# Kernel optimization log

Measured on AMD Instinct MI355X. Metric: run time of the kernel, lower is better.

The kernel has to match this reference:

```python
import jax, jax.numpy as jnp
import numpy as np

N = 100_000      # num nodes
E = 100_000      # num hyperedges
NNZ = 1_600_000  # incidence entries (avg degree 16)
DIN = 128
DOUT = 128


def setup_inputs() -> dict:
    key = jax.random.key(0)
    k1, k2, k3, k4 = jax.random.split(key, 4)
    x = jax.random.normal(k1, (N, DIN), dtype=jnp.float32)
    weight = jax.random.normal(k2, (DIN, DOUT), dtype=jnp.float32) / np.sqrt(DIN).astype(np.float32)
    bias = jax.random.normal(k3, (DOUT,), dtype=jnp.float32) * 0.02
    hyperedge_index = jax.random.randint(k4, (2, NNZ), 0, N, dtype=jnp.int64)
    return {"x": x, "weight": weight, "bias": bias, "hyperedge_index": hyperedge_index}


def reference(x, weight, bias, hyperedge_index):
    # PyG HypergraphConv (use_attention=False, heads=1):
    #   out = D^{-1} H W B^{-1} H^T (x @ Theta) + bias, W = I (unit hyperedge weights)
    node_idx = hyperedge_index[0]  # [NNZ]
    edge_idx = hyperedge_index[1]  # [NNZ]

    h = x @ weight  # [N, DOUT]

    ones = jnp.ones((NNZ,), dtype=h.dtype)
    # node degree D_i = sum of hyperedge weights (=1) over incident hyperedges
    D = jax.ops.segment_sum(ones, node_idx, num_segments=N)   # [N]
    # hyperedge degree B_e = number of incident nodes
    B = jax.ops.segment_sum(ones, edge_idx, num_segments=E)   # [E]
    Dinv = jnp.where(D > 0, 1.0 / D, 0.0)
    Binv = jnp.where(B > 0, 1.0 / B, 0.0)

    # nodes -> hyperedges: m_e = B_e^{-1} * sum_{i in e} h_i
    e_feat = jax.ops.segment_sum(h[node_idx], edge_idx, num_segments=E) * Binv[:, None]  # [E, DOUT]
    # hyperedges -> nodes: out_i = D_i^{-1} * sum_{e ni i} m_e
    out = jax.ops.segment_sum(e_feat[edge_idx], node_idx, num_segments=N) * Dinv[:, None]  # [N, DOUT]
    return out + bias
```

## Files before the change

### kernel.cpp

```cpp
#include <hip/hip_runtime.h>

#define Nn 100000
#define Ne 100000
#define NNZC 1600000
#define NBLK 256
#define CHUNK 6250
#define BSH 8
#define BUCKW 256
#define NBK 391
#define GEMM_BLOCKS 1563

typedef __attribute__((ext_vector_type(8))) short short8;
typedef __attribute__((ext_vector_type(4))) float floatx4;

__device__ inline unsigned short f2bf(float f) {
    union { float f; unsigned int i; } c; c.f = f;
    unsigned int i = c.i;
    return (unsigned short)((i + 0x7fffu + ((i >> 16) & 1u)) >> 16);
}
__device__ inline unsigned int f2bf2(float lo, float hi) {
    union { float f; unsigned int i; } a, b;
    a.f = lo; b.f = hi;
    const unsigned int x = (a.i + 0x7fffu + ((a.i >> 16) & 1u)) >> 16;
    const unsigned int y = (b.i + 0x7fffu + ((b.i >> 16) & 1u)) & 0xffff0000u;
    return x | y;
}

__global__ void hist_kernel(const int* __restrict__ nidx, const int* __restrict__ eidx,
                            int* __restrict__ histN, int* __restrict__ histE) {
    __shared__ int hN[NBK], hE[NBK];
    for (int j = threadIdx.x; j < NBK; j += 256) { hN[j] = 0; hE[j] = 0; }
    __syncthreads();
    const int base = blockIdx.x * CHUNK;
    for (int i = base + threadIdx.x; i < base + CHUNK; i += 256) {
        atomicAdd(&hN[nidx[i] >> BSH], 1);
        atomicAdd(&hE[eidx[i] >> BSH], 1);
    }
    __syncthreads();
    for (int j = threadIdx.x; j < NBK; j += 256) {
        histN[j * NBLK + blockIdx.x] = hN[j];
        histE[j * NBLK + blockIdx.x] = hE[j];
    }
}

__global__ void scan1_kernel(int* __restrict__ histN, int* __restrict__ histE,
                             int* __restrict__ bsumN, int* __restrict__ bsumE) {
    const int arr = blockIdx.x / NBK;
    const int b = blockIdx.x % NBK;
    int* a = arr ? histE : histN;
    int* bs = arr ? bsumE : bsumN;
    const int t = threadIdx.x;
    int v = a[b * 256 + t];
    __shared__ int tmp[2][256];
    int pin = 0;
    tmp[0][t] = v;
    for (int off = 1; off < 256; off <<= 1) {
        __syncthreads();
        int val = tmp[pin][t];
        if (t >= off) val += tmp[pin][t - off];
        tmp[1 - pin][t] = val;
        pin ^= 1;
    }
    __syncthreads();
    int incl = tmp[pin][t];
    a[b * 256 + t] = incl - v;
    if (t == 255) bs[b] = incl;
}

__global__ void scan3_kernel(int* __restrict__ histN, int* __restrict__ histE,
                             const int* __restrict__ bsumN, const int* __restrict__ bsumE) {
    const int arr = blockIdx.x / NBK;
    const int b = blockIdx.x % NBK;
    int* a = arr ? histE : histN;
    const int* bs = arr ? bsumE : bsumN;
    const int t = threadIdx.x;
    int part = 0;
    for (int i = t; i < b; i += 256) part += bs[i];
    __shared__ int red[256];
    red[t] = part;
    __syncthreads();
    for (int off = 128; off > 0; off >>= 1) {
        if (t < off) red[t] += red[t + off];
        __syncthreads();
    }
    a[b * 256 + t] += red[0];
}

__global__ __launch_bounds__(256) void gemm_scatter_kernel(
        const float* __restrict__ x, const float* __restrict__ w,
        unsigned short* __restrict__ h,
        const int* __restrict__ nidx, const int* __restrict__ eidx,
        const int* __restrict__ histN, const int* __restrict__ histE,
        unsigned int* __restrict__ pairsN, unsigned int* __restrict__ pairsE) {
    __shared__ union {
        struct { unsigned short wlds[128 * 136]; unsigned short tile[4][16 * 136]; } g;
        struct { int cN[NBK]; int cE[NBK]; } s;
    } sm;
    const int tid = threadIdx.x;

    if (blockIdx.x < GEMM_BLOCKS) {
        const int wave = tid >> 6, lane = tid & 63;
        const int q = lane >> 4, r16 = lane & 15;

        for (int i = tid; i < 4096; i += 256) {
            const int k = i >> 5;
            const int n0 = (i & 31) << 2;
            const float4 wv = *(const float4*)(w + k * 128 + n0);
            sm.g.wlds[(n0 + 0) * 136 + k] = f2bf(wv.x);
            sm.g.wlds[(n0 + 1) * 136 + k] = f2bf(wv.y);
            sm.g.wlds[(n0 + 2) * 136 + k] = f2bf(wv.z);
            sm.g.wlds[(n0 + 3) * 136 + k] = f2bf(wv.w);
        }
        __syncthreads();

        const int row0 = blockIdx.x * 64 + wave * 16;
        if (row0 >= Nn) return;

        floatx4 acc[8];
#pragma unroll
        for (int jb = 0; jb < 8; ++jb) acc[jb] = (floatx4){0.f, 0.f, 0.f, 0.f};

        const float* ap = x + (size_t)(row0 + r16) * 128 + q * 8;
#pragma unroll
        for (int kk = 0; kk < 4; ++kk) {
            const float4 a0 = *(const float4*)(ap + kk * 32);
            const float4 a1 = *(const float4*)(ap + kk * 32 + 4);
            union { unsigned int u[4]; short8 s; } af;
            af.u[0] = f2bf2(a0.x, a0.y);
            af.u[1] = f2bf2(a0.z, a0.w);
            af.u[2] = f2bf2(a1.x, a1.y);
            af.u[3] = f2bf2(a1.z, a1.w);
            const unsigned short* wp = sm.g.wlds + kk * 32 + q * 8;
#pragma unroll
            for (int jb = 0; jb < 8; ++jb) {
                const short8 bfr = *(const short8*)(wp + (jb * 16 + r16) * 136);
                acc[jb] = __builtin_amdgcn_mfma_f32_16x16x32_bf16(af.s, bfr, acc[jb], 0, 0, 0);
            }
        }

        unsigned short* tw = sm.g.tile[wave];
#pragma unroll
        for (int jb = 0; jb < 8; ++jb)
#pragma unroll
            for (int r = 0; r < 4; ++r)
                tw[(q * 4 + r) * 136 + jb * 16 + r16] = f2bf(acc[jb][r]);

        const int rr = lane >> 2, seg = lane & 3;
        const unsigned short* src = tw + rr * 136 + seg * 32;
        unsigned short* dst = h + (size_t)(row0 + rr) * 128 + seg * 32;
        *(short8*)(dst + 0)  = *(const short8*)(src + 0);
        *(short8*)(dst + 8)  = *(const short8*)(src + 8);
        *(short8*)(dst + 16) = *(const short8*)(src + 16);
        *(short8*)(dst + 24) = *(const short8*)(src + 24);
    } else {
        const int blk = blockIdx.x - GEMM_BLOCKS;
        for (int j = tid; j < NBK; j += 256) {
            sm.s.cN[j] = histN[j * NBLK + blk];
            sm.s.cE[j] = histE[j * NBLK + blk];
        }
        __syncthreads();
        const int base = blk * CHUNK;
        for (int i = base + tid; i < base + CHUNK; i += 256) {
            const int n = nidx[i], e = eidx[i];
            const int pn = atomicAdd(&sm.s.cN[n >> BSH], 1);
            const int pe = atomicAdd(&sm.s.cE[e >> BSH], 1);
            pairsN[pn] = ((unsigned int)e << 8) | (unsigned int)(n & 255);
            pairsE[pe] = ((unsigned int)n << 8) | (unsigned int)(e & 255);
        }
    }
}

__global__ void fine_kernel(const unsigned int* __restrict__ pairsN, const unsigned int* __restrict__ pairsE,
                            const int* __restrict__ histN, const int* __restrict__ histE,
                            int* __restrict__ offsN, int* __restrict__ offsE,
                            int* __restrict__ permN, int* __restrict__ permE) {
    const int arr = blockIdx.x / NBK;
    const int b = blockIdx.x % NBK;
    const unsigned int* pairs = arr ? pairsE : pairsN;
    const int* hist = arr ? histE : histN;
    int* offs = arr ? offsE : offsN;
    int* perm = arr ? permE : permN;
    const int t = threadIdx.x;
    const int S = hist[b * NBLK];
    const int E = (b + 1 < NBK) ? hist[(b + 1) * NBLK] : NNZC;
    __shared__ int cnt[BUCKW];
    __shared__ int tmp[2][BUCKW];
    cnt[t] = 0;
    __syncthreads();
    for (int i = S + t; i < E; i += BUCKW)
        atomicAdd(&cnt[pairs[i] & 255u], 1);
    __syncthreads();
    int v = cnt[t];
    int pin = 0;
    tmp[0][t] = v;
    for (int off = 1; off < BUCKW; off <<= 1) {
        __syncthreads();
        int val = tmp[pin][t];
        if (t >= off) val += tmp[pin][t - off];
        tmp[1 - pin][t] = val;
        pin ^= 1;
    }
    __syncthreads();
    const int excl = tmp[pin][t] - v;
    const int id = b * BUCKW + t;
    if (id < 100000) offs[id] = S + excl;
    if (b == NBK - 1 && t == 0) offs[100000] = NNZC;
    __syncthreads();
    cnt[t] = excl;
    __syncthreads();
    for (int i = S + t; i < E; i += BUCKW) {
        const unsigned int p = pairs[i];
        const int pos = S + atomicAdd(&cnt[p & 255u], 1);
        perm[pos] = (int)(p >> 8);
    }
}

__device__ inline void gather_rows(const char* __restrict__ src, const int* __restrict__ perm,
                                   int start, int end, int lane, float& ax, float& ay) {
    const unsigned int laneoff = (unsigned int)lane << 2;
    for (int s0 = start; s0 < end; s0 += 64) {
        const int m = min(end - s0, 64);
        const int myv = perm[s0 + (lane < m ? lane : 0)];
        int t = 0;
        for (; t + 7 < m; t += 8) {
            unsigned int a[8], u[8];
#pragma unroll
            for (int j = 0; j < 8; ++j)
                a[j] = ((unsigned int)__shfl(myv, t + j, 64) << 8) | laneoff;
#pragma unroll
            for (int j = 0; j < 8; ++j) u[j] = *(const unsigned int*)(src + a[j]);
#pragma unroll
            for (int j = 0; j < 8; ++j) {
                ax += __uint_as_float(u[j] << 16);
                ay += __uint_as_float(u[j] & 0xffff0000u);
            }
        }
        if (t < m) {
            unsigned int a[8], u[8];
            float f[8];
#pragma unroll
            for (int j = 0; j < 8; ++j) {
                const int idx = (t + j < m) ? t + j : t;
                f[j] = (t + j < m) ? 1.f : 0.f;
                a[j] = ((unsigned int)__shfl(myv, idx, 64) << 8) | laneoff;
            }
#pragma unroll
            for (int j = 0; j < 8; ++j) u[j] = *(const unsigned int*)(src + a[j]);
#pragma unroll
            for (int j = 0; j < 8; ++j) {
                ax += f[j] * __uint_as_float(u[j] << 16);
                ay += f[j] * __uint_as_float(u[j] & 0xffff0000u);
            }
        }
    }
}

__global__ void gather_n2e_kernel(const int* __restrict__ perm, const int* __restrict__ offs,
                                  const unsigned short* __restrict__ h,
                                  unsigned short* __restrict__ ef) {
    const int wave = threadIdx.x >> 6;
    const int lane = threadIdx.x & 63;
    const int e = blockIdx.x * 4 + wave;
    const int start = offs[e], end = offs[e + 1];
    float ax = 0.f, ay = 0.f;
    gather_rows((const char*)h, perm, start, end, lane, ax, ay);
    const int deg = end - start;
    const float binv = deg ? 1.f / (float)deg : 0.f;
    const unsigned int o = f2bf2(ax * binv, ay * binv);
    *(unsigned int*)((char*)ef + (((unsigned int)e << 8) | ((unsigned int)lane << 2))) = o;
}

__global__ void gather_e2n_kernel(const int* __restrict__ perm, const int* __restrict__ offs,
                                  const unsigned short* __restrict__ ef,
                                  const float* __restrict__ bias,
                                  float* __restrict__ out) {
    const int wave = threadIdx.x >> 6;
    const int lane = threadIdx.x & 63;
    const int n = blockIdx.x * 4 + wave;
    const int start = offs[n], end = offs[n + 1];
    float ax = 0.f, ay = 0.f;
    gather_rows((const char*)ef, perm, start, end, lane, ax, ay);
    const int deg = end - start;
    const float dinv = deg ? 1.f / (float)deg : 0.f;
    const float2 b = ((const float2*)bias)[lane];
    float2 o;
    o.x = ax * dinv + b.x;
    o.y = ay * dinv + b.y;
    *(float2*)((char*)out + (((unsigned int)n << 9) | ((unsigned int)lane << 3))) = o;
}

extern "C" void kernel_launch(void* const* d_in, const int* in_sizes, int n_in,
                              void* d_out, int out_size, void* d_ws, size_t ws_size,
                              hipStream_t stream) {
    const float* x = (const float*)d_in[0];
    const float* w = (const float*)d_in[1];
    const float* bias = (const float*)d_in[2];
    const int* hei = (const int*)d_in[3];
    const int* nidx = hei;
    const int* eidx = hei + NNZC;
    float* out = (float*)d_out;

    char* p = (char*)d_ws;
    unsigned short* h = (unsigned short*)p;  p += (size_t)Nn * 128 * 2;
    unsigned short* ef = (unsigned short*)p; p += (size_t)Ne * 128 * 2;
    int* histN = (int*)p;                    p += (size_t)NBK * NBLK * 4 + 256;
    int* histE = (int*)p;                    p += (size_t)NBK * NBLK * 4 + 256;
    int* bsumN = (int*)p;                    p += 1792;
    int* bsumE = (int*)p;                    p += 1792;
    int* offsN = (int*)p;                    p += 400128;
    int* offsE = (int*)p;                    p += 400128;
    int* permN = (int*)p;                    p += (size_t)NNZC * 4;
    int* permE = (int*)p;                    p += (size_t)NNZC * 4;
    unsigned int* pairsN = (unsigned int*)p; p += (size_t)NNZC * 4;
    unsigned int* pairsE = (unsigned int*)p; p += (size_t)NNZC * 4;

    hist_kernel<<<NBLK, 256, 0, stream>>>(nidx, eidx, histN, histE);
    scan1_kernel<<<2 * NBK, 256, 0, stream>>>(histN, histE, bsumN, bsumE);
    scan3_kernel<<<2 * NBK, 256, 0, stream>>>(histN, histE, bsumN, bsumE);
    gemm_scatter_kernel<<<GEMM_BLOCKS + NBLK, 256, 0, stream>>>(
        x, w, h, nidx, eidx, histN, histE, pairsN, pairsE);
    fine_kernel<<<2 * NBK, BUCKW, 0, stream>>>(pairsN, pairsE, histN, histE,
                                               offsN, offsE, permN, permE);

    gather_n2e_kernel<<<Ne / 4, 256, 0, stream>>>(permE, offsE, h, ef);
    gather_e2n_kernel<<<Nn / 4, 256, 0, stream>>>(permN, offsN, ef, bias, out);
}
```

Measured before the change: 313.1 us.

## Split GEMM across histogram and scatter kernels, cache bucket pairs in LDS

The GEMM blocks are now split in half. One half runs alongside the histogram pass and the other alongside the scatter pass, so the light memory-bound kernels overlap with compute. The GEMM epilogue swaps MFMA operand order and writes bf16 results straight to global memory, dropping the LDS transpose tile and shrinking shared memory. The fine sort kernel caches the bucket's pairs in LDS on its first pass so the second pass avoids reloading them from global memory, at the cost of more LDS per block.

After: 299.8 us. -4.2%, faster.

```diff
diff --git a/kernel.cpp b/kernel.cpp
--- a/kernel.cpp
+++ b/kernel.cpp
@@ -8,7 +8,10 @@
 #define BSH 8
 #define BUCKW 256
 #define NBK 391
-#define GEMM_BLOCKS 1563
+#define GEMM_TOTAL 1563
+#define GEMM_A 782
+#define GEMM_B 781
+#define FCAP 5888
 
 typedef __attribute__((ext_vector_type(8))) short short8;
 typedef __attribute__((ext_vector_type(4))) float floatx4;
@@ -26,20 +29,88 @@
     return x | y;
 }
 
-__global__ void hist_kernel(const int* __restrict__ nidx, const int* __restrict__ eidx,
-                            int* __restrict__ histN, int* __restrict__ histE) {
-    __shared__ int hN[NBK], hE[NBK];
-    for (int j = threadIdx.x; j < NBK; j += 256) { hN[j] = 0; hE[j] = 0; }
-    __syncthreads();
-    const int base = blockIdx.x * CHUNK;
-    for (int i = base + threadIdx.x; i < base + CHUNK; i += 256) {
-        atomicAdd(&hN[nidx[i] >> BSH], 1);
-        atomicAdd(&hE[eidx[i] >> BSH], 1);
-    }
-    __syncthreads();
-    for (int j = threadIdx.x; j < NBK; j += 256) {
-        histN[j * NBLK + blockIdx.x] = hN[j];
-        histE[j * NBLK + blockIdx.x] = hE[j];
+union FusedLds {
+    unsigned short wlds[128 * 136];
+    struct { int a[NBK]; int b[NBK]; } s;
+};
+
+__device__ inline void gemm_block(int gb, const float* __restrict__ x,
+                                  const float* __restrict__ w,
+                                  unsigned short* __restrict__ h,
+                                  unsigned short* wlds, int tid) {
+    const int wave = tid >> 6, lane = tid & 63;
+    const int q = lane >> 4, r16 = lane & 15;
+
+    for (int i = tid; i < 4096; i += 256) {
+        const int k = i >> 5;
+        const int n0 = (i & 31) << 2;
+        const float4 wv = *(const float4*)(w + k * 128 + n0);
+        wlds[(n0 + 0) * 136 + k] = f2bf(wv.x);
+        wlds[(n0 + 1) * 136 + k] = f2bf(wv.y);
+        wlds[(n0 + 2) * 136 + k] = f2bf(wv.z);
+        wlds[(n0 + 3) * 136 + k] = f2bf(wv.w);
+    }
+    __syncthreads();
+
+    const int row0 = gb * 64 + wave * 16;
+    const int rrow = min(row0 + r16, Nn - 1);
+
+    floatx4 acc[8];
+#pragma unroll
+    for (int jb = 0; jb < 8; ++jb) acc[jb] = (floatx4){0.f, 0.f, 0.f, 0.f};
+
+    const float* ap = x + (size_t)rrow * 128 + q * 8;
+#pragma unroll
+    for (int kk = 0; kk < 4; ++kk) {
+        const float4 a0 = *(const float4*)(ap + kk * 32);
+        const float4 a1 = *(const float4*)(ap + kk * 32 + 4);
+        union { unsigned int u[4]; short8 s; } xf;
+        xf.u[0] = f2bf2(a0.x, a0.y);
+        xf.u[1] = f2bf2(a0.z, a0.w);
+        xf.u[2] = f2bf2(a1.x, a1.y);
+        xf.u[3] = f2bf2(a1.z, a1.w);
+        const unsigned short* wp = wlds + kk * 32 + q * 8;
+#pragma unroll
+        for (int jb = 0; jb < 8; ++jb) {
+            const short8 wf = *(const short8*)(wp + (jb * 16 + r16) * 136);
+            acc[jb] = __builtin_amdgcn_mfma_f32_16x16x32_bf16(wf, xf.s, acc[jb], 0, 0, 0);
+        }
+    }
+
+    if (row0 + r16 < Nn) {
+        unsigned short* hb = h + (size_t)(row0 + r16) * 128 + q * 4;
+#pragma unroll
+        for (int jb = 0; jb < 8; ++jb) {
+            uint2 o;
+            o.x = f2bf2(acc[jb][0], acc[jb][1]);
+            o.y = f2bf2(acc[jb][2], acc[jb][3]);
+            *(uint2*)(hb + jb * 16) = o;
+        }
+    }
+}
+
+__global__ __launch_bounds__(256) void hist_gemm_kernel(
+        const int* __restrict__ nidx, const int* __restrict__ eidx,
+        int* __restrict__ histN, int* __restrict__ histE,
+        const float* __restrict__ x, const float* __restrict__ w,
+        unsigned short* __restrict__ h) {
+    __shared__ FusedLds sm;
+    const int tid = threadIdx.x;
+    if (blockIdx.x < NBLK) {
+        for (int j = tid; j < NBK; j += 256) { sm.s.a[j] = 0; sm.s.b[j] = 0; }
+        __syncthreads();
+        const int base = blockIdx.x * CHUNK;
+        for (int i = base + tid; i < base + CHUNK; i += 256) {
+            atomicAdd(&sm.s.a[nidx[i] >> BSH], 1);
+            atomicAdd(&sm.s.b[eidx[i] >> BSH], 1);
+        }
+        __syncthreads();
+        for (int j = tid; j < NBK; j += 256) {
+            histN[j * NBLK + blockIdx.x] = sm.s.a[j];
+            histE[j * NBLK + blockIdx.x] = sm.s.b[j];
+        }
+    } else {
+        gemm_block(blockIdx.x - NBLK, x, w, h, sm.wlds, tid);
     }
 }
 
@@ -86,87 +157,31 @@
     a[b * 256 + t] += red[0];
 }
 
-__global__ __launch_bounds__(256) void gemm_scatter_kernel(
-        const float* __restrict__ x, const float* __restrict__ w,
-        unsigned short* __restrict__ h,
+__global__ __launch_bounds__(256) void scatter_gemm_kernel(
         const int* __restrict__ nidx, const int* __restrict__ eidx,
         const int* __restrict__ histN, const int* __restrict__ histE,
-        unsigned int* __restrict__ pairsN, unsigned int* __restrict__ pairsE) {
-    __shared__ union {
-        struct { unsigned short wlds[128 * 136]; unsigned short tile[4][16 * 136]; } g;
-        struct { int cN[NBK]; int cE[NBK]; } s;
-    } sm;
+        unsigned int* __restrict__ pairsN, unsigned int* __restrict__ pairsE,
+        const float* __restrict__ x, const float* __restrict__ w,
+        unsigned short* __restrict__ h) {
+    __shared__ FusedLds sm;
     const int tid = threadIdx.x;
-
-    if (blockIdx.x < GEMM_BLOCKS) {
-        const int wave = tid >> 6, lane = tid & 63;
-        const int q = lane >> 4, r16 = lane & 15;
-
-        for (int i = tid; i < 4096; i += 256) {
-            const int k = i >> 5;
-            const int n0 = (i & 31) << 2;
-            const float4 wv = *(const float4*)(w + k * 128 + n0);
-            sm.g.wlds[(n0 + 0) * 136 + k] = f2bf(wv.x);
-            sm.g.wlds[(n0 + 1) * 136 + k] = f2bf(wv.y);
-            sm.g.wlds[(n0 + 2) * 136 + k] = f2bf(wv.z);
-            sm.g.wlds[(n0 + 3) * 136 + k] = f2bf(wv.w);
-        }
-        __syncthreads();
-
-        const int row0 = blockIdx.x * 64 + wave * 16;
-        if (row0 >= Nn) return;
-
-        floatx4 acc[8];
-#pragma unroll
-        for (int jb = 0; jb < 8; ++jb) acc[jb] = (floatx4){0.f, 0.f, 0.f, 0.f};
-
-        const float* ap = x + (size_t)(row0 + r16) * 128 + q * 8;
-#pragma unroll
-        for (int kk = 0; kk < 4; ++kk) {
-            const float4 a0 = *(const float4*)(ap + kk * 32);
-            const float4 a1 = *(const float4*)(ap + kk * 32 + 4);
-            union { unsigned int u[4]; short8 s; } af;
-            af.u[0] = f2bf2(a0.x, a0.y);
-            af.u[1] = f2bf2(a0.z, a0.w);
-            af.u[2] = f2bf2(a1.x, a1.y);
-            af.u[3] = f2bf2(a1.z, a1.w);
-            const unsigned short* wp = sm.g.wlds + kk * 32 + q * 8;
-#pragma unroll
-            for (int jb = 0; jb < 8; ++jb) {
-                const short8 bfr = *(const short8*)(wp + (jb * 16 + r16) * 136);
-                acc[jb] = __builtin_amdgcn_mfma_f32_16x16x32_bf16(af.s, bfr, acc[jb], 0, 0, 0);
-            }
-        }
-
-        unsigned short* tw = sm.g.tile[wave];
-#pragma unroll
-        for (int jb = 0; jb < 8; ++jb)
-#pragma unroll
-            for (int r = 0; r < 4; ++r)
-                tw[(q * 4 + r) * 136 + jb * 16 + r16] = f2bf(acc[jb][r]);
-
-        const int rr = lane >> 2, seg = lane & 3;
-        const unsigned short* src = tw + rr * 136 + seg * 32;
-        unsigned short* dst = h + (size_t)(row0 + rr) * 128 + seg * 32;
-        *(short8*)(dst + 0)  = *(const short8*)(src + 0);
-        *(short8*)(dst + 8)  = *(const short8*)(src + 8);
-        *(short8*)(dst + 16) = *(const short8*)(src + 16);
-        *(short8*)(dst + 24) = *(const short8*)(src + 24);
-    } else {
-        const int blk = blockIdx.x - GEMM_BLOCKS;
+    if (blockIdx.x < NBLK) {
+        const int blk = blockIdx.x;
         for (int j = tid; j < NBK; j += 256) {
-            sm.s.cN[j] = histN[j * NBLK + blk];
-            sm.s.cE[j] = histE[j * NBLK + blk];
+            sm.s.a[j] = histN[j * NBLK + blk];
+            sm.s.b[j] = histE[j * NBLK + blk];
         }
         __syncthreads();
         const int base = blk * CHUNK;
         for (int i = base + tid; i < base + CHUNK; i += 256) {
             const int n = nidx[i], e = eidx[i];
-            const int pn = atomicAdd(&sm.s.cN[n >> BSH], 1);
-            const int pe = atomicAdd(&sm.s.cE[e >> BSH], 1);
+            const int pn = atomicAdd(&sm.s.a[n >> BSH], 1);
+            const int pe = atomicAdd(&sm.s.b[e >> BSH], 1);
             pairsN[pn] = ((unsigned int)e << 8) | (unsigned int)(n & 255);
             pairsE[pe] = ((unsigned int)n << 8) | (unsigned int)(e & 255);
         }
+    } else {
+        gemm_block(GEMM_A + blockIdx.x - NBLK, x, w, h, sm.wlds, tid);
     }
 }
 
@@ -185,10 +200,15 @@
     const int E = (b + 1 < NBK) ? hist[(b + 1) * NBLK] : NNZC;
     __shared__ int cnt[BUCKW];
     __shared__ int tmp[2][BUCKW];
+    __shared__ unsigned int cache[FCAP];
     cnt[t] = 0;
     __syncthreads();
-    for (int i = S + t; i < E; i += BUCKW)
-        atomicAdd(&cnt[pairs[i] & 255u], 1);
+    for (int i = S + t; i < E; i += BUCKW) {
+        const unsigned int p = pairs[i];
+        const int loc = i - S;
+        if (loc < FCAP) cache[loc] = p;
+        atomicAdd(&cnt[p & 255u], 1);
+    }
     __syncthreads();
     int v = cnt[t];
     int pin = 0;
@@ -209,7 +229,8 @@
     cnt[t] = excl;
     __syncthreads();
     for (int i = S + t; i < E; i += BUCKW) {
-        const unsigned int p = pairs[i];
+        const int loc = i - S;
+        const unsigned int p = (loc < FCAP) ? cache[loc] : pairs[i];
         const int pos = S + atomicAdd(&cnt[p & 255u], 1);
         perm[pos] = (int)(p >> 8);
     }
@@ -314,11 +335,11 @@
     unsigned int* pairsN = (unsigned int*)p; p += (size_t)NNZC * 4;
     unsigned int* pairsE = (unsigned int*)p; p += (size_t)NNZC * 4;
 
-    hist_kernel<<<NBLK, 256, 0, stream>>>(nidx, eidx, histN, histE);
+    hist_gemm_kernel<<<NBLK + GEMM_A, 256, 0, stream>>>(nidx, eidx, histN, histE, x, w, h);
     scan1_kernel<<<2 * NBK, 256, 0, stream>>>(histN, histE, bsumN, bsumE);
     scan3_kernel<<<2 * NBK, 256, 0, stream>>>(histN, histE, bsumN, bsumE);
-    gemm_scatter_kernel<<<GEMM_BLOCKS + NBLK, 256, 0, stream>>>(
-        x, w, h, nidx, eidx, histN, histE, pairsN, pairsE);
+    scatter_gemm_kernel<<<NBLK + GEMM_B, 256, 0, stream>>>(nidx, eidx, histN, histE,
+                                                           pairsN, pairsE, x, w, h);
     fine_kernel<<<2 * NBK, BUCKW, 0, stream>>>(pairsN, pairsE, histN, histE,
                                                offsN, offsE, permN, permE);
 
```
